# Kernel tuning notes

Hardware: AMD Instinct MI355X
Metric: run time of the kernel (lower is better)

## Reference

```python
import jax, jax.numpy as jnp
import numpy as np

B, T, D, K = 64, 512, 1024, 50


def setup_inputs() -> dict:
    key = jax.random.key(0)
    ks = jax.random.split(key, 6)
    inputs = jax.random.normal(ks[0], (B, T, D), dtype=jnp.float32)
    mask = jnp.ones((B, T), dtype=jnp.int32)
    labels = jax.random.randint(ks[1], (B, T), 0, K)
    W = jax.random.normal(ks[2], (D, K), dtype=jnp.float32) / jnp.sqrt(jnp.float32(D))
    b = jnp.zeros((K,), dtype=jnp.float32)
    transitions = jax.random.normal(ks[3], (K, K), dtype=jnp.float32) * 0.1
    start_transitions = jax.random.normal(ks[4], (K,), dtype=jnp.float32) * 0.1
    end_transitions = jax.random.normal(ks[5], (K,), dtype=jnp.float32) * 0.1
    return dict(inputs=inputs, mask=mask, labels=labels, W=W, b=b,
                transitions=transitions, start_transitions=start_transitions,
                end_transitions=end_transitions)


def _log_partition(emissions, mask_f, trans, start, end):
    # emissions [B,T,K]; forward algorithm with logsumexp recurrence (lax.scan)
    alpha0 = start[None, :] + emissions[:, 0]  # [B,K]
    def step(alpha, xs):
        emit, m = xs  # [B,K], [B]
        inner = alpha[:, :, None] + trans[None, :, :] + emit[:, None, :]  # [B,K,K]
        new = jax.nn.logsumexp(inner, axis=1)
        alpha = jnp.where(m[:, None] > 0, new, alpha)  # carry state through padding
        return alpha, None
    emits = jnp.swapaxes(emissions[:, 1:], 0, 1)  # [T-1,B,K]
    ms = jnp.swapaxes(mask_f[:, 1:], 0, 1)
    alpha, _ = jax.lax.scan(step, alpha0, (emits, ms))
    return jax.nn.logsumexp(alpha + end[None, :], axis=1)  # [B]


def _gold_score(emissions, labels, mask_f, trans, start, end):
    emit_sc = jnp.take_along_axis(emissions, labels[..., None], axis=2)[..., 0]  # [B,T]
    emit_sum = jnp.sum(emit_sc * mask_f, axis=1)
    trans_sc = trans[labels[:, :-1], labels[:, 1:]]  # [B,T-1]
    trans_sum = jnp.sum(trans_sc * mask_f[:, 1:], axis=1)
    last_idx = jnp.sum(mask_f, axis=1).astype(jnp.int32) - 1
    last_tags = jnp.take_along_axis(labels, last_idx[:, None], axis=1)[:, 0]
    return start[labels[:, 0]] + emit_sum + trans_sum + end[last_tags]


def _viterbi(emissions, mask_f, trans, start, end):
    Bv, Tv, Kv = emissions.shape
    alpha0 = start[None, :] + emissions[:, 0]
    ident = jnp.broadcast_to(jnp.arange(Kv, dtype=jnp.int32)[None, :], (Bv, Kv))
    def step(alpha, xs):
        emit, m = xs
        inner = alpha[:, :, None] + trans[None, :, :]  # [B,K_prev,K_cur]
        bp = jnp.argmax(inner, axis=1).astype(jnp.int32)  # [B,K]
        new = jnp.max(inner, axis=1) + emit
        cond = m[:, None] > 0
        alpha = jnp.where(cond, new, alpha)
        bp = jnp.where(cond, bp, ident)  # padded step: tag carries through
        return alpha, bp
    emits = jnp.swapaxes(emissions[:, 1:], 0, 1)
    ms = jnp.swapaxes(mask_f[:, 1:], 0, 1)
    alpha, bps = jax.lax.scan(step, alpha0, (emits, ms))  # bps [T-1,B,K]
    last = jnp.argmax(alpha + end[None, :], axis=1).astype(jnp.int32)  # [B]
    def back(tag, bp):
        prev = jnp.take_along_axis(bp, tag[:, None], axis=1)[:, 0]
        return prev, tag
    first_tag, tags_rest = jax.lax.scan(back, last, bps, reverse=True)  # tags_rest[t]=tag at pos t+1
    tags = jnp.concatenate([first_tag[None, :], tags_rest], axis=0)  # [T,B]
    return jnp.swapaxes(tags, 0, 1)  # [B,T]


def reference(inputs, mask, labels, W, b, transitions, start_transitions, end_transitions):
    emissions = inputs @ W + b  # tag_projection: [B,T,K]
    mask_f = mask.astype(emissions.dtype)
    scores = emissions * mask_f[..., None]  # module masks logits before CRF
    tags = _viterbi(scores, mask_f, transitions, start_transitions, end_transitions)
    tags = tags * mask.astype(tags.dtype)
    ll = _gold_score(scores, labels, mask_f, transitions, start_transitions, end_transitions) \
         - _log_partition(scores, mask_f, transitions, start_transitions, end_transitions)
    loss = -jnp.sum(ll)  # reduction='sum' negative log-likelihood
    return scores, tags, loss
```

## Files before the change

### kernel.cpp

```cpp
#include <hip/hip_runtime.h>

#define B_ 64
#define T_ 512
#define D_ 1024
#define K_ 50
#define MROWS (B_ * T_)

__global__ __launch_bounds__(256) void gemm_kernel(const float* __restrict__ A,
                                                   const float* __restrict__ W,
                                                   float* __restrict__ P0,
                                                   float* __restrict__ P1) {
  __shared__ float As[128][20];
  __shared__ float Wt[52][20];

  const int tid = threadIdx.x;
  const int rowBase = blockIdx.x * 128;
  const int kBase = blockIdx.y * 512;
  float* __restrict__ P = blockIdx.y ? P1 : P0;

  const int rg = tid & 63;
  const int cg = tid >> 6;
  const int c0 = cg * 13;
  const int swr = (rg >> 3) & 3;

  float acc[2][13];
#pragma unroll
  for (int i = 0; i < 2; i++)
#pragma unroll
    for (int j = 0; j < 13; j++) acc[i][j] = 0.f;

  const int q = tid & 3;
  const int rr = tid >> 2;

  for (int ch = 0; ch < 32; ++ch) {
    const int kb = kBase + (ch << 4);
#pragma unroll
    for (int s = 0; s < 2; s++) {
      const int r = rr + 64 * s;
      const float4 v = *(const float4*)&A[(size_t)(rowBase + r) * 1024 + kb + q * 4];
      const int p = (q + ((r >> 3) & 3)) & 3;
      *(float4*)&As[r][p * 4] = v;
    }
#pragma unroll
    for (int s = 0; s < 4; s++) {
      const int l = tid + 256 * s;
      if (l < 832) {
        const int kk = l / 52;
        const int c = l - kk * 52;
        Wt[c][kk] = (c < 50) ? W[(size_t)(kb + kk) * 50 + c] : 0.f;
      }
    }
    __syncthreads();
#pragma unroll
    for (int k4 = 0; k4 < 4; k4++) {
      const int pq = ((k4 + swr) & 3) * 4;
      const float4 a0 = *(const float4*)&As[rg][pq];
      const float4 a1 = *(const float4*)&As[rg + 64][pq];
#pragma unroll
      for (int j = 0; j < 13; j++) {
        const float4 w = *(const float4*)&Wt[c0 + j][k4 * 4];
        float t0 = acc[0][j], t1 = acc[1][j];
        t0 = fmaf(a0.x, w.x, t0); t1 = fmaf(a1.x, w.x, t1);
        t0 = fmaf(a0.y, w.y, t0); t1 = fmaf(a1.y, w.y, t1);
        t0 = fmaf(a0.z, w.z, t0); t1 = fmaf(a1.z, w.z, t1);
        t0 = fmaf(a0.w, w.w, t0); t1 = fmaf(a1.w, w.w, t1);
        acc[0][j] = t0; acc[1][j] = t1;
      }
    }
    __syncthreads();
  }
#pragma unroll
  for (int j = 0; j < 13; j++) {
    const int c = c0 + j;
    if (c < 50) {
      P[(size_t)(rowBase + rg) * 50 + c] = acc[0][j];
      P[(size_t)(rowBase + rg + 64) * 50 + c] = acc[1][j];
    }
  }
}

__global__ __launch_bounds__(256) void combine_kernel(const float* __restrict__ P1,
                                                      const float* __restrict__ bias,
                                                      const int* __restrict__ mask,
                                                      float* __restrict__ scores,
                                                      float* __restrict__ lossSlot) {
  const int idx = blockIdx.x * 256 + threadIdx.x;
  const int m = idx / 50;
  const int c = idx - m * 50;
  const float v = (scores[idx] + P1[idx] + bias[c]) * (float)mask[m];
  scores[idx] = v;
  if (idx == 0) *lossSlot = 0.f;
}

__global__ __launch_bounds__(256) void crf_kernel(const float* __restrict__ scores,
                                                  const int* __restrict__ mask,
                                                  const int* __restrict__ labels,
                                                  const float* __restrict__ trans,
                                                  const float* __restrict__ startT,
                                                  const float* __restrict__ endT,
                                                  float* __restrict__ tagsOut,
                                                  float* __restrict__ lossSlot) {
  __shared__ float x_lds[64];
  __shared__ unsigned char bp_s[511 * 52];
  __shared__ unsigned char g_s[32 * 52];
  __shared__ unsigned char chin_s[32];
  __shared__ float redp_s[4];
  __shared__ int redm_s[4];
  __shared__ float logZ_s;
  __shared__ int last_s;

  const int b = blockIdx.x;
  const int tid = threadIdx.x;
  const int wave = tid >> 6;
  const int lane = tid & 63;
  const int k = lane;
  const int kc = (k < 50) ? k : 49;
  const size_t sb = (size_t)b * T_ * 50;
  const int bT = b * T_;

  if (blockIdx.y == 0) {
    if (wave == 0) {
      float4 eTv[13];
#pragma unroll
      for (int u = 0; u < 13; u++) {
        const int j = 4 * u;
        eTv[u].x = (j + 0 < 50) ? __expf(trans[(j + 0) * 50 + kc]) : 0.f;
        eTv[u].y = (j + 1 < 50) ? __expf(trans[(j + 1) * 50 + kc]) : 0.f;
        eTv[u].z = (j + 2 < 50) ? __expf(trans[(j + 2) * 50 + kc]) : 0.f;
        eTv[u].w = (j + 3 < 50) ? __expf(trans[(j + 3) * 50 + kc]) : 0.f;
      }
      float af = (k < 50) ? (startT[k] + scores[sb + k]) : -1e30f;
      float M = __int_as_float(__builtin_amdgcn_readfirstlane(__float_as_int(af)));
      float em0 = scores[sb + 50 + kc];
      float em1 = scores[sb + 100 + kc];
      int mk0 = mask[bT + 1];
      int mk1 = mask[bT + 2];
      for (int t = 1; t < T_; ++t) {
        const float emit = em0;
        const int mt = mk0;
        em0 = em1; mk0 = mk1;
        if (t + 2 < T_) {
          em1 = scores[sb + (size_t)(t + 2) * 50 + kc];
          mk1 = mask[bT + t + 2];
        }
        const float e = __expf(af - M);
        x_lds[lane] = e;
        float p0 = 0.f, p1 = 0.f, p2 = 0.f, p3 = 0.f;
#pragma unroll
        for (int u = 0; u < 13; u++) {
          const float4 w = *(const float4*)&x_lds[4 * u];
          p0 = fmaf(w.x, eTv[u].x, p0);
          p1 = fmaf(w.y, eTv[u].y, p1);
          p2 = fmaf(w.z, eTv[u].z, p2);
          p3 = fmaf(w.w, eTv[u].w, p3);
        }
        const float S = (p0 + p1) + (p2 + p3);
        const float afn = M + __logf(S) + emit;
        af = (mt > 0 && k < 50) ? afn : af;
        M = __int_as_float(__builtin_amdgcn_readfirstlane(__float_as_int(af)));
      }
      const float x = (k < 50) ? (af + endT[k]) : -3e38f;
      float mx = x;
#pragma unroll
      for (int off = 32; off >= 1; off >>= 1) mx = fmaxf(mx, __shfl_xor(mx, off));
      float sm = (k < 50) ? __expf(x - mx) : 0.f;
#pragma unroll
      for (int off = 32; off >= 1; off >>= 1) sm += __shfl_xor(sm, off);
      if (lane == 0) logZ_s = mx + __logf(sm);
    } else {
      float part = 0.f;
      int mcnt = 0;
#pragma unroll
      for (int s = 0; s < 3; s++) {
        const int t = (tid - 64) + 192 * s;
        if (t < T_) {
          const int lt = labels[bT + t];
          const int mt = mask[bT + t];
          mcnt += mt;
          if (mt > 0) part += scores[sb + (size_t)t * 50 + lt];
          if (t < T_ - 1) {
            const int ln = labels[bT + t + 1];
            const int mn = mask[bT + t + 1];
            if (mn > 0) part += trans[lt * 50 + ln];
          }
        }
      }
#pragma unroll
      for (int off = 32; off >= 1; off >>= 1) {
        part += __shfl_xor(part, off);
        mcnt += __shfl_xor(mcnt, off);
      }
      if (lane == 0) { redp_s[wave] = part; redm_s[wave] = mcnt; }
    }
    __syncthreads();
    if (tid == 0) {
      float gold = redp_s[1] + redp_s[2] + redp_s[3];
      const int tot = redm_s[1] + redm_s[2] + redm_s[3];
      const int l0 = labels[bT];
      const int llast = labels[bT + (tot - 1)];
      gold += startT[l0] + endT[llast];
      atomicAdd(lossSlot, -(gold - logZ_s));
    }
  } else {
    if (wave == 0) {
      float4 Tv[13];
#pragma unroll
      for (int u = 0; u < 13; u++) {
        const int j = 4 * u;
        Tv[u].x = (j + 0 < 50) ? trans[(j + 0) * 50 + kc] : -1e30f;
        Tv[u].y = (j + 1 < 50) ? trans[(j + 1) * 50 + kc] : -1e30f;
        Tv[u].z = (j + 2 < 50) ? trans[(j + 2) * 50 + kc] : -1e30f;
        Tv[u].w = (j + 3 < 50) ? trans[(j + 3) * 50 + kc] : -1e30f;
      }
      float av = (k < 50) ? (startT[k] + scores[sb + k]) : -1e30f;
      float em0 = scores[sb + 50 + kc];
      float em1 = scores[sb + 100 + kc];
      int mk0 = mask[bT + 1];
      int mk1 = mask[bT + 2];
      for (int t = 1; t < T_; ++t) {
        const float emit = em0;
        const int mt = mk0;
        em0 = em1; mk0 = mk1;
        if (t + 2 < T_) {
          em1 = scores[sb + (size_t)(t + 2) * 50 + kc];
          mk1 = mask[bT + t + 2];
        }
        x_lds[lane] = av;
        float4 u0, u1, u2, u3, u4, u5, u6, u7, u8, u9, u10, u11, u12;
        float m13[13];
#define VIT_QUAD(Q, UQ)                                            \
        {                                                          \
          const float4 w = *(const float4*)&x_lds[4 * (Q)];        \
          UQ.x = w.x + Tv[Q].x; UQ.y = w.y + Tv[Q].y;              \
          UQ.z = w.z + Tv[Q].z; UQ.w = w.w + Tv[Q].w;              \
          m13[Q] = fmaxf(fmaxf(UQ.x, UQ.y), fmaxf(UQ.z, UQ.w));    \
        }
        VIT_QUAD(0, u0)   VIT_QUAD(1, u1)   VIT_QUAD(2, u2)
        VIT_QUAD(3, u3)   VIT_QUAD(4, u4)   VIT_QUAD(5, u5)
        VIT_QUAD(6, u6)   VIT_QUAD(7, u7)   VIT_QUAD(8, u8)
        VIT_QUAD(9, u9)   VIT_QUAD(10, u10) VIT_QUAD(11, u11)
        VIT_QUAD(12, u12)
#undef VIT_QUAD
        const float h0 = fmaxf(m13[0], m13[1]);
        const float h1 = fmaxf(m13[2], m13[3]);
        const float h2 = fmaxf(m13[4], m13[5]);
        const float h3 = fmaxf(m13[6], m13[7]);
        const float h4 = fmaxf(m13[8], m13[9]);
        const float h5 = fmaxf(m13[10], m13[11]);
        const float best = fmaxf(fmaxf(fmaxf(h0, h1), fmaxf(h2, h3)),
                                 fmaxf(fmaxf(h4, h5), m13[12]));
        int bj = 0;
#define VIT_SCAN(Q, UQ)                                   \
        bj = (UQ.w == best) ? 4 * (Q) + 3 : bj;           \
        bj = (UQ.z == best) ? 4 * (Q) + 2 : bj;           \
        bj = (UQ.y == best) ? 4 * (Q) + 1 : bj;           \
        bj = (UQ.x == best) ? 4 * (Q) + 0 : bj;
        VIT_SCAN(12, u12) VIT_SCAN(11, u11) VIT_SCAN(10, u10)
        VIT_SCAN(9, u9)   VIT_SCAN(8, u8)   VIT_SCAN(7, u7)
        VIT_SCAN(6, u6)   VIT_SCAN(5, u5)   VIT_SCAN(4, u4)
        VIT_SCAN(3, u3)   VIT_SCAN(2, u2)   VIT_SCAN(1, u1)
        VIT_SCAN(0, u0)
#undef VIT_SCAN
        if (k < 50) bp_s[(t - 1) * 52 + k] = (unsigned char)((mt > 0) ? bj : k);
        av = (mt > 0 && k < 50) ? (best + emit) : av;
      }
      float x = (k < 50) ? (av + endT[k]) : -3e38f;
      int xi = (k < 50) ? k : 63;
#pragma unroll
      for (int off = 32; off >= 1; off >>= 1) {
        const float ov = __shfl_xor(x, off);
        const int oi = __shfl_xor(xi, off);
        if (ov > x || (ov == x && oi < xi)) { x = ov; xi = oi; }
      }
      if (lane == 0) last_s = xi;
    }
    __syncthreads();
    const int last = last_s;
    for (int p = 0; p < 7; p++) {
      const int idx = tid + 256 * p;
      if (idx < 1600) {
        const int c = idx / 50;
        const int s2 = idx - c * 50;
        int x2 = s2;
        const int lo = 16 * c;
        const int hi = min(16 * c + 15, 510);
        for (int i = hi; i >= lo; --i) x2 = bp_s[i * 52 + x2];
        g_s[c * 52 + s2] = (unsigned char)x2;
      }
    }
    __syncthreads();
    if (tid == 0) {
      int cur = last;
      chin_s[31] = (unsigned char)cur;
      for (int c = 31; c >= 1; --c) {
        cur = g_s[c * 52 + cur];
        chin_s[c - 1] = (unsigned char)cur;
      }
      const int m511 = mask[bT + 511];
      tagsOut[(size_t)bT + 511] = (float)((m511 > 0) ? last : 0);
    }
    __syncthreads();
    if (tid < 32) {
      const int c = tid;
      int x3 = chin_s[c];
      const int lo = 16 * c;
      const int hi = min(16 * c + 15, 510);
      for (int i = hi; i >= lo; --i) {
        x3 = bp_s[i * 52 + x3];
        const int mi = mask[bT + i];
        tagsOut[(size_t)bT + i] = (float)((mi > 0) ? x3 : 0);
      }
    }
  }
}

extern "C" void kernel_launch(void* const* d_in, const int* in_sizes, int n_in,
                              void* d_out, int out_size, void* d_ws, size_t ws_size,
                              hipStream_t stream) {
  const float* inputs = (const float*)d_in[0];
  const int* mask = (const int*)d_in[1];
  const int* labels = (const int*)d_in[2];
  const float* W = (const float*)d_in[3];
  const float* bias = (const float*)d_in[4];
  const float* trans = (const float*)d_in[5];
  const float* startT = (const float*)d_in[6];
  const float* endT = (const float*)d_in[7];

  float* out = (float*)d_out;
  float* scores = out;
  float* tagsOut = out + (size_t)B_ * T_ * K_;
  float* lossSlot = out + (size_t)B_ * T_ * K_ + B_ * T_;
  float* P1 = (float*)d_ws;

  dim3 g1(MROWS / 128, 2);
  gemm_kernel<<<g1, 256, 0, stream>>>(inputs, W, scores, P1);

  combine_kernel<<<(K_ * MROWS) / 256, 256, 0, stream>>>(P1, bias, mask, scores,
                                                         lossSlot);

  dim3 g3(B_, 2);
  crf_kernel<<<g3, 256, 0, stream>>>(scores, mask, labels, trans, startT, endT,
                                     tagsOut, lossSlot);
}
```

Before: 663.9 us.

## Retile GEMM to 4x7 per thread with register prefetch; split CRF into single-wave blocks

The GEMM now gives each thread 4 rows by 7 columns instead of 2 by 13, which changes the mix of LDS reads and FMAs. Global loads for the next k-chunk are prefetched into registers so their latency overlaps the current chunk's compute. The CRF kernel now launches one 64-thread wave per block, and the gold-score reduction moves to its own third block row that adds its contribution to the loss atomically. The forward and Viterbi waves no longer share a block with idle waves, and transition vectors are pinned in registers with inline asm, at the cost of more total blocks and one more atomic per batch row.

```diff
diff --git a/kernel.cpp b/kernel.cpp
--- a/kernel.cpp
+++ b/kernel.cpp
@@ -18,63 +18,86 @@
   const int kBase = blockIdx.y * 512;
   float* __restrict__ P = blockIdx.y ? P1 : P0;
 
-  const int rg = tid & 63;
-  const int cg = tid >> 6;
-  const int c0 = cg * 13;
+  const int rg = tid & 31;
+  const int cg = tid >> 5;
+  const int c0 = cg * 7;
   const int swr = (rg >> 3) & 3;
-
-  float acc[2][13];
-#pragma unroll
-  for (int i = 0; i < 2; i++)
-#pragma unroll
-    for (int j = 0; j < 13; j++) acc[i][j] = 0.f;
 
   const int q = tid & 3;
   const int rr = tid >> 2;
+  const int pA0 = ((q + ((rr >> 3) & 3)) & 3) * 4;
+  const int pA1 = ((q + (((rr + 64) >> 3) & 3)) & 3) * 4;
+  const int kk0 = tid / 52,         cw0 = tid - kk0 * 52;
+  const int kk1 = (tid + 256) / 52, cw1 = tid + 256 - kk1 * 52;
+  const int kk2 = (tid + 512) / 52, cw2 = tid + 512 - kk2 * 52;
+  const int kk3 = (tid + 768) / 52, cw3 = tid + 768 - kk3 * 52;
+
+  float acc[4][7];
+#pragma unroll
+  for (int i = 0; i < 4; i++)
+#pragma unroll
+    for (int j = 0; j < 7; j++) acc[i][j] = 0.f;
+
+  const float* __restrict__ pA0g = &A[(size_t)(rowBase + rr) * 1024 + kBase + q * 4];
+  const float* __restrict__ pA1g = &A[(size_t)(rowBase + rr + 64) * 1024 + kBase + q * 4];
+  const float* __restrict__ pWg = &W[(size_t)kBase * 50];
+
+  float4 nA0 = *(const float4*)pA0g;
+  float4 nA1 = *(const float4*)pA1g;
+  float nW0 = (cw0 < 50) ? pWg[(size_t)kk0 * 50 + cw0] : 0.f;
+  float nW1 = (cw1 < 50) ? pWg[(size_t)kk1 * 50 + cw1] : 0.f;
+  float nW2 = (cw2 < 50) ? pWg[(size_t)kk2 * 50 + cw2] : 0.f;
+  float nW3 = (tid < 64 && cw3 < 50) ? pWg[(size_t)kk3 * 50 + cw3] : 0.f;
 
   for (int ch = 0; ch < 32; ++ch) {
-    const int kb = kBase + (ch << 4);
-#pragma unroll
-    for (int s = 0; s < 2; s++) {
-      const int r = rr + 64 * s;
-      const float4 v = *(const float4*)&A[(size_t)(rowBase + r) * 1024 + kb + q * 4];
-      const int p = (q + ((r >> 3) & 3)) & 3;
-      *(float4*)&As[r][p * 4] = v;
-    }
-#pragma unroll
-    for (int s = 0; s < 4; s++) {
-      const int l = tid + 256 * s;
-      if (l < 832) {
-        const int kk = l / 52;
-        const int c = l - kk * 52;
-        Wt[c][kk] = (c < 50) ? W[(size_t)(kb + kk) * 50 + c] : 0.f;
-      }
-    }
-    __syncthreads();
+    *(float4*)&As[rr][pA0] = nA0;
+    *(float4*)&As[rr + 64][pA1] = nA1;
+    Wt[cw0][kk0] = nW0;
+    Wt[cw1][kk1] = nW1;
+    Wt[cw2][kk2] = nW2;
+    if (tid < 64) Wt[cw3][kk3] = nW3;
+    __syncthreads();
+    if (ch < 31) {
+      const int off = (ch + 1) * 16;
+      nA0 = *(const float4*)(pA0g + off);
+      nA1 = *(const float4*)(pA1g + off);
+      const float* pw = pWg + (size_t)off * 50;
+      nW0 = (cw0 < 50) ? pw[(size_t)kk0 * 50 + cw0] : 0.f;
+      nW1 = (cw1 < 50) ? pw[(size_t)kk1 * 50 + cw1] : 0.f;
+      nW2 = (cw2 < 50) ? pw[(size_t)kk2 * 50 + cw2] : 0.f;
+      nW3 = (tid < 64 && cw3 < 50) ? pw[(size_t)kk3 * 50 + cw3] : 0.f;
+    }
 #pragma unroll
     for (int k4 = 0; k4 < 4; k4++) {
       const int pq = ((k4 + swr) & 3) * 4;
       const float4 a0 = *(const float4*)&As[rg][pq];
-      const float4 a1 = *(const float4*)&As[rg + 64][pq];
-#pragma unroll
-      for (int j = 0; j < 13; j++) {
+      const float4 a1 = *(const float4*)&As[rg + 32][pq];
+      const float4 a2 = *(const float4*)&As[rg + 64][pq];
+      const float4 a3 = *(const float4*)&As[rg + 96][pq];
+#pragma unroll
+      for (int j = 0; j < 7; j++) {
         const float4 w = *(const float4*)&Wt[c0 + j][k4 * 4];
-        float t0 = acc[0][j], t1 = acc[1][j];
+        float t0 = acc[0][j], t1 = acc[1][j], t2 = acc[2][j], t3 = acc[3][j];
         t0 = fmaf(a0.x, w.x, t0); t1 = fmaf(a1.x, w.x, t1);
+        t2 = fmaf(a2.x, w.x, t2); t3 = fmaf(a3.x, w.x, t3);
         t0 = fmaf(a0.y, w.y, t0); t1 = fmaf(a1.y, w.y, t1);
+        t2 = fmaf(a2.y, w.y, t2); t3 = fmaf(a3.y, w.y, t3);
         t0 = fmaf(a0.z, w.z, t0); t1 = fmaf(a1.z, w.z, t1);
+        t2 = fmaf(a2.z, w.z, t2); t3 = fmaf(a3.z, w.z, t3);
         t0 = fmaf(a0.w, w.w, t0); t1 = fmaf(a1.w, w.w, t1);
-        acc[0][j] = t0; acc[1][j] = t1;
+        t2 = fmaf(a2.w, w.w, t2); t3 = fmaf(a3.w, w.w, t3);
+        acc[0][j] = t0; acc[1][j] = t1; acc[2][j] = t2; acc[3][j] = t3;
       }
     }
     __syncthreads();
   }
 #pragma unroll
-  for (int j = 0; j < 13; j++) {
+  for (int j = 0; j < 7; j++) {
     const int c = c0 + j;
     if (c < 50) {
-      P[(size_t)(rowBase + rg) * 50 + c] = acc[0][j];
-      P[(size_t)(rowBase + rg + 64) * 50 + c] = acc[1][j];
+#pragma unroll
+      for (int i = 0; i < 4; i++)
+        P[(size_t)(rowBase + rg + 32 * i) * 50 + c] = acc[i][j];
     }
   }
 }
@@ -92,204 +115,163 @@
   if (idx == 0) *lossSlot = 0.f;
 }
 
-__global__ __launch_bounds__(256) void crf_kernel(const float* __restrict__ scores,
-                                                  const int* __restrict__ mask,
-                                                  const int* __restrict__ labels,
-                                                  const float* __restrict__ trans,
-                                                  const float* __restrict__ startT,
-                                                  const float* __restrict__ endT,
-                                                  float* __restrict__ tagsOut,
-                                                  float* __restrict__ lossSlot) {
+#define PIN4(V) asm volatile("" : "+v"(V.x), "+v"(V.y), "+v"(V.z), "+v"(V.w))
+
+__global__ __launch_bounds__(64, 1) void crf_kernel(const float* __restrict__ scores,
+                                                    const int* __restrict__ mask,
+                                                    const int* __restrict__ labels,
+                                                    const float* __restrict__ trans,
+                                                    const float* __restrict__ startT,
+                                                    const float* __restrict__ endT,
+                                                    float* __restrict__ tagsOut,
+                                                    float* __restrict__ lossSlot) {
   __shared__ float x_lds[64];
   __shared__ unsigned char bp_s[511 * 52];
   __shared__ unsigned char g_s[32 * 52];
   __shared__ unsigned char chin_s[32];
-  __shared__ float redp_s[4];
-  __shared__ int redm_s[4];
-  __shared__ float logZ_s;
-  __shared__ int last_s;
 
   const int b = blockIdx.x;
-  const int tid = threadIdx.x;
-  const int wave = tid >> 6;
-  const int lane = tid & 63;
+  const int lane = threadIdx.x;
   const int k = lane;
   const int kc = (k < 50) ? k : 49;
   const size_t sb = (size_t)b * T_ * 50;
   const int bT = b * T_;
 
   if (blockIdx.y == 0) {
-    if (wave == 0) {
-      float4 eTv[13];
+    float4 eTv[13];
+#pragma unroll
+    for (int u = 0; u < 13; u++) {
+      const int j = 4 * u;
+      eTv[u].x = (j + 0 < 50) ? __expf(trans[(j + 0) * 50 + kc]) : 0.f;
+      eTv[u].y = (j + 1 < 50) ? __expf(trans[(j + 1) * 50 + kc]) : 0.f;
+      eTv[u].z = (j + 2 < 50) ? __expf(trans[(j + 2) * 50 + kc]) : 0.f;
+      eTv[u].w = (j + 3 < 50) ? __expf(trans[(j + 3) * 50 + kc]) : 0.f;
+      PIN4(eTv[u]);
+    }
+    float af = (k < 50) ? (startT[k] + scores[sb + k]) : -1e30f;
+    float M = __int_as_float(__builtin_amdgcn_readfirstlane(__float_as_int(af)));
+    float em0 = scores[sb + 50 + kc];
+    float em1 = scores[sb + 100 + kc];
+    int mk0 = mask[bT + 1];
+    int mk1 = mask[bT + 2];
+    for (int t = 1; t < T_; ++t) {
+      const float emit = em0;
+      const int mt = mk0;
+      em0 = em1; mk0 = mk1;
+      if (t + 2 < T_) {
+        em1 = scores[sb + (size_t)(t + 2) * 50 + kc];
+        mk1 = mask[bT + t + 2];
+      }
+      const float e = __expf(af - M);
+      x_lds[lane] = e;
+      float p0 = 0.f, p1 = 0.f, p2 = 0.f, p3 = 0.f;
 #pragma unroll
       for (int u = 0; u < 13; u++) {
-        const int j = 4 * u;
-        eTv[u].x = (j + 0 < 50) ? __expf(trans[(j + 0) * 50 + kc]) : 0.f;
-        eTv[u].y = (j + 1 < 50) ? __expf(trans[(j + 1) * 50 + kc]) : 0.f;
-        eTv[u].z = (j + 2 < 50) ? __expf(trans[(j + 2) * 50 + kc]) : 0.f;
-        eTv[u].w = (j + 3 < 50) ? __expf(trans[(j + 3) * 50 + kc]) : 0.f;
-      }
-      float af = (k < 50) ? (startT[k] + scores[sb + k]) : -1e30f;
-      float M = __int_as_float(__builtin_amdgcn_readfirstlane(__float_as_int(af)));
-      float em0 = scores[sb + 50 + kc];
-      float em1 = scores[sb + 100 + kc];
-      int mk0 = mask[bT + 1];
-      int mk1 = mask[bT + 2];
-      for (int t = 1; t < T_; ++t) {
-        const float emit = em0;
-        const int mt = mk0;
-        em0 = em1; mk0 = mk1;
-        if (t + 2 < T_) {
-          em1 = scores[sb + (size_t)(t + 2) * 50 + kc];
-          mk1 = mask[bT + t + 2];
-        }
-        const float e = __expf(af - M);
-        x_lds[lane] = e;
-        float p0 = 0.f, p1 = 0.f, p2 = 0.f, p3 = 0.f;
-#pragma unroll
-        for (int u = 0; u < 13; u++) {
-          const float4 w = *(const float4*)&x_lds[4 * u];
-          p0 = fmaf(w.x, eTv[u].x, p0);
-          p1 = fmaf(w.y, eTv[u].y, p1);
-          p2 = fmaf(w.z, eTv[u].z, p2);
-          p3 = fmaf(w.w, eTv[u].w, p3);
-        }
-        const float S = (p0 + p1) + (p2 + p3);
-        const float afn = M + __logf(S) + emit;
-        af = (mt > 0 && k < 50) ? afn : af;
-        M = __int_as_float(__builtin_amdgcn_readfirstlane(__float_as_int(af)));
-      }
-      const float x = (k < 50) ? (af + endT[k]) : -3e38f;
-      float mx = x;
-#pragma unroll
-      for (int off = 32; off >= 1; off >>= 1) mx = fmaxf(mx, __shfl_xor(mx, off));
-      float sm = (k < 50) ? __expf(x - mx) : 0.f;
-#pragma unroll
-      for (int off = 32; off >= 1; off >>= 1) sm += __shfl_xor(sm, off);
-      if (lane == 0) logZ_s = mx + __logf(sm);
-    } else {
-      float part = 0.f;
-      int mcnt = 0;
-#pragma unroll
-      for (int s = 0; s < 3; s++) {
-        const int t = (tid - 64) + 192 * s;
-        if (t < T_) {
-          const int lt = labels[bT + t];
-          const int mt = mask[bT + t];
-          mcnt += mt;
-          if (mt > 0) part += scores[sb + (size_t)t * 50 + lt];
-          if (t < T_ - 1) {
-            const int ln = labels[bT + t + 1];
-            const int mn = mask[bT + t + 1];
-            if (mn > 0) part += trans[lt * 50 + ln];
-          }
-        }
-      }
-#pragma unroll
-      for (int off = 32; off >= 1; off >>= 1) {
-        part += __shfl_xor(part, off);
-        mcnt += __shfl_xor(mcnt, off);
-      }
-      if (lane == 0) { redp_s[wave] = part; redm_s[wave] = mcnt; }
-    }
-    __syncthreads();
-    if (tid == 0) {
-      float gold = redp_s[1] + redp_s[2] + redp_s[3];
-      const int tot = redm_s[1] + redm_s[2] + redm_s[3];
-      const int l0 = labels[bT];
-      const int llast = labels[bT + (tot - 1)];
-      gold += startT[l0] + endT[llast];
-      atomicAdd(lossSlot, -(gold - logZ_s));
-    }
-  } else {
-    if (wave == 0) {
-      float4 Tv[13];
-#pragma unroll
-      for (int u = 0; u < 13; u++) {
-        const int j = 4 * u;
-        Tv[u].x = (j + 0 < 50) ? trans[(j + 0) * 50 + kc] : -1e30f;
-        Tv[u].y = (j + 1 < 50) ? trans[(j + 1) * 50 + kc] : -1e30f;
-        Tv[u].z = (j + 2 < 50) ? trans[(j + 2) * 50 + kc] : -1e30f;
-        Tv[u].w = (j + 3 < 50) ? trans[(j + 3) * 50 + kc] : -1e30f;
-      }
-      float av = (k < 50) ? (startT[k] + scores[sb + k]) : -1e30f;
-      float em0 = scores[sb + 50 + kc];
-      float em1 = scores[sb + 100 + kc];
-      int mk0 = mask[bT + 1];
-      int mk1 = mask[bT + 2];
-      for (int t = 1; t < T_; ++t) {
-        const float emit = em0;
-        const int mt = mk0;
-        em0 = em1; mk0 = mk1;
-        if (t + 2 < T_) {
-          em1 = scores[sb + (size_t)(t + 2) * 50 + kc];
-          mk1 = mask[bT + t + 2];
-        }
-        x_lds[lane] = av;
-        float4 u0, u1, u2, u3, u4, u5, u6, u7, u8, u9, u10, u11, u12;
-        float m13[13];
+        const float4 w = *(const float4*)&x_lds[4 * u];
+        p0 = fmaf(w.x, eTv[u].x, p0);
+        p1 = fmaf(w.y, eTv[u].y, p1);
+        p2 = fmaf(w.z, eTv[u].z, p2);
+        p3 = fmaf(w.w, eTv[u].w, p3);
+      }
+      const float S = (p0 + p1) + (p2 + p3);
+      const float afn = M + __logf(S) + emit;
+      af = (mt > 0 && k < 50) ? afn : af;
+      M = __int_as_float(__builtin_amdgcn_readfirstlane(__float_as_int(af)));
+    }
+    const float x = (k < 50) ? (af + endT[k]) : -3e38f;
+    float mx = x;
+#pragma unroll
+    for (int off = 32; off >= 1; off >>= 1) mx = fmaxf(mx, __shfl_xor(mx, off));
+    float sm = (k < 50) ? __expf(x - mx) : 0.f;
+#pragma unroll
+    for (int off = 32; off >= 1; off >>= 1) sm += __shfl_xor(sm, off);
+    if (lane == 0) atomicAdd(lossSlot, mx + __logf(sm));
+  } else if (blockIdx.y == 1) {
+    float4 Tv[13];
+#pragma unroll
+    for (int u = 0; u < 13; u++) {
+      const int j = 4 * u;
+      Tv[u].x = (j + 0 < 50) ? trans[(j + 0) * 50 + kc] : -1e30f;
+      Tv[u].y = (j + 1 < 50) ? trans[(j + 1) * 50 + kc] : -1e30f;
+      Tv[u].z = (j + 2 < 50) ? trans[(j + 2) * 50 + kc] : -1e30f;
+      Tv[u].w = (j + 3 < 50) ? trans[(j + 3) * 50 + kc] : -1e30f;
+      PIN4(Tv[u]);
+    }
+    float av = (k < 50) ? (startT[k] + scores[sb + k]) : -1e30f;
+    float em0 = scores[sb + 50 + kc];
+    float em1 = scores[sb + 100 + kc];
+    int mk0 = mask[bT + 1];
+    int mk1 = mask[bT + 2];
+    for (int t = 1; t < T_; ++t) {
+      const float emit = em0;
+      const int mt = mk0;
+      em0 = em1; mk0 = mk1;
+      if (t + 2 < T_) {
+        em1 = scores[sb + (size_t)(t + 2) * 50 + kc];
+        mk1 = mask[bT + t + 2];
+      }
+      x_lds[lane] = av;
+      float4 u0, u1, u2, u3, u4, u5, u6, u7, u8, u9, u10, u11, u12;
+      float m13[13];
 #define VIT_QUAD(Q, UQ)                                            \
-        {                                                          \
-          const float4 w = *(const float4*)&x_lds[4 * (Q)];        \
-          UQ.x = w.x + Tv[Q].x; UQ.y = w.y + Tv[Q].y;              \
-          UQ.z = w.z + Tv[Q].z; UQ.w = w.w + Tv[Q].w;              \
-          m13[Q] = fmaxf(fmaxf(UQ.x, UQ.y), fmaxf(UQ.z, UQ.w));    \
-        }
-        VIT_QUAD(0, u0)   VIT_QUAD(1, u1)   VIT_QUAD(2, u2)
-        VIT_QUAD(3, u3)   VIT_QUAD(4, u4)   VIT_QUAD(5, u5)
-        VIT_QUAD(6, u6)   VIT_QUAD(7, u7)   VIT_QUAD(8, u8)
-        VIT_QUAD(9, u9)   VIT_QUAD(10, u10) VIT_QUAD(11, u11)
-        VIT_QUAD(12, u12)
+      {                                                            \
+        const float4 w = *(const float4*)&x_lds[4 * (Q)];          \
+        UQ.x = w.x + Tv[Q].x; UQ.y = w.y + Tv[Q].y;                \
+        UQ.z = w.z + Tv[Q].z; UQ.w = w.w + Tv[Q].w;                \
+        m13[Q] = fmaxf(fmaxf(UQ.x, UQ.y), fmaxf(UQ.z, UQ.w));      \
+      }
+      VIT_QUAD(0, u0)   VIT_QUAD(1, u1)   VIT_QUAD(2, u2)
+      VIT_QUAD(3, u3)   VIT_QUAD(4, u4)   VIT_QUAD(5, u5)
+      VIT_QUAD(6, u6)   VIT_QUAD(7, u7)   VIT_QUAD(8, u8)
+      VIT_QUAD(9, u9)   VIT_QUAD(10, u10) VIT_QUAD(11, u11)
+      VIT_QUAD(12, u12)
 #undef VIT_QUAD
-        const float h0 = fmaxf(m13[0], m13[1]);
-        const float h1 = fmaxf(m13[2], m13[3]);
-        const float h2 = fmaxf(m13[4], m13[5]);
-        const float h3 = fmaxf(m13[6], m13[7]);
-        const float h4 = fmaxf(m13[8], m13[9]);
-        const float h5 = fmaxf(m13[10], m13[11]);
-        const float best = fmaxf(fmaxf(fmaxf(h0, h1), fmaxf(h2, h3)),
-                                 fmaxf(fmaxf(h4, h5), m13[12]));
-        int bj = 0;
+      const float h0 = fmaxf(m13[0], m13[1]);
+      const float h1 = fmaxf(m13[2], m13[3]);
+      const float h2 = fmaxf(m13[4], m13[5]);
+      const float h3 = fmaxf(m13[6], m13[7]);
+      const float h4 = fmaxf(m13[8], m13[9]);
+      const float h5 = fmaxf(m13[10], m13[11]);
+      const float best = fmaxf(fmaxf(fmaxf(h0, h1), fmaxf(h2, h3)),
+                               fmaxf(fmaxf(h4, h5), m13[12]));
+      int bj = 0;
 #define VIT_SCAN(Q, UQ)                                   \
-        bj = (UQ.w == best) ? 4 * (Q) + 3 : bj;           \
-        bj = (UQ.z == best) ? 4 * (Q) + 2 : bj;           \
-        bj = (UQ.y == best) ? 4 * (Q) + 1 : bj;           \
-        bj = (UQ.x == best) ? 4 * (Q) + 0 : bj;
-        VIT_SCAN(12, u12) VIT_SCAN(11, u11) VIT_SCAN(10, u10)
-        VIT_SCAN(9, u9)   VIT_SCAN(8, u8)   VIT_SCAN(7, u7)
-        VIT_SCAN(6, u6)   VIT_SCAN(5, u5)   VIT_SCAN(4, u4)
-        VIT_SCAN(3, u3)   VIT_SCAN(2, u2)   VIT_SCAN(1, u1)
-        VIT_SCAN(0, u0)
+      bj = (UQ.w == best) ? 4 * (Q) + 3 : bj;             \
+      bj = (UQ.z == best) ? 4 * (Q) + 2 : bj;             \
+      bj = (UQ.y == best) ? 4 * (Q) + 1 : bj;             \
+      bj = (UQ.x == best) ? 4 * (Q) + 0 : bj;
+      VIT_SCAN(12, u12) VIT_SCAN(11, u11) VIT_SCAN(10, u10)
+      VIT_SCAN(9, u9)   VIT_SCAN(8, u8)   VIT_SCAN(7, u7)
+      VIT_SCAN(6, u6)   VIT_SCAN(5, u5)   VIT_SCAN(4, u4)
+      VIT_SCAN(3, u3)   VIT_SCAN(2, u2)   VIT_SCAN(1, u1)
+      VIT_SCAN(0, u0)
 #undef VIT_SCAN
-        if (k < 50) bp_s[(t - 1) * 52 + k] = (unsigned char)((mt > 0) ? bj : k);
-        av = (mt > 0 && k < 50) ? (best + emit) : av;
-      }
-      float x = (k < 50) ? (av + endT[k]) : -3e38f;
-      int xi = (k < 50) ? k : 63;
-#pragma unroll
-      for (int off = 32; off >= 1; off >>= 1) {
-        const float ov = __shfl_xor(x, off);
-        const int oi = __shfl_xor(xi, off);
-        if (ov > x || (ov == x && oi < xi)) { x = ov; xi = oi; }
-      }
-      if (lane == 0) last_s = xi;
-    }
-    __syncthreads();
-    const int last = last_s;
-    for (int p = 0; p < 7; p++) {
-      const int idx = tid + 256 * p;
-      if (idx < 1600) {
-        const int c = idx / 50;
-        const int s2 = idx - c * 50;
-        int x2 = s2;
-        const int lo = 16 * c;
-        const int hi = min(16 * c + 15, 510);
-        for (int i = hi; i >= lo; --i) x2 = bp_s[i * 52 + x2];
-        g_s[c * 52 + s2] = (unsigned char)x2;
-      }
-    }
-    __syncthreads();
-    if (tid == 0) {
+      if (k < 50) bp_s[(t - 1) * 52 + k] = (unsigned char)((mt > 0) ? bj : k);
+      av = (mt > 0 && k < 50) ? (best + emit) : av;
+    }
+    float x = (k < 50) ? (av + endT[k]) : -3e38f;
+    int xi = (k < 50) ? k : 63;
+#pragma unroll
+    for (int off = 32; off >= 1; off >>= 1) {
+      const float ov = __shfl_xor(x, off);
+      const int oi = __shfl_xor(xi, off);
+      if (ov > x || (ov == x && oi < xi)) { x = ov; xi = oi; }
+    }
+    const int last = xi;
+    __syncthreads();
+#pragma unroll 1
+    for (int p = 0; p < 25; p++) {
+      const int idx = lane + 64 * p;
+      const int c = idx / 50;
+      const int s2 = idx - c * 50;
+      int x2 = s2;
+      const int lo = 16 * c;
+      const int hi = min(16 * c + 15, 510);
+      for (int i = hi; i >= lo; --i) x2 = bp_s[i * 52 + x2];
+      g_s[c * 52 + s2] = (unsigned char)x2;
+    }
+    __syncthreads();
+    if (lane == 0) {
       int cur = last;
       chin_s[31] = (unsigned char)cur;
       for (int c = 31; c >= 1; --c) {
@@ -300,8 +282,8 @@
       tagsOut[(size_t)bT + 511] = (float)((m511 > 0) ? last : 0);
     }
     __syncthreads();
-    if (tid < 32) {
-      const int c = tid;
+    if (lane < 32) {
+      const int c = lane;
       int x3 = chin_s[c];
       const int lo = 16 * c;
       const int hi = min(16 * c + 15, 510);
@@ -310,6 +292,33 @@
         const int mi = mask[bT + i];
         tagsOut[(size_t)bT + i] = (float)((mi > 0) ? x3 : 0);
       }
+    }
+  } else {
+    float part = 0.f;
+    int mcnt = 0;
+#pragma unroll
+    for (int s = 0; s < 8; s++) {
+      const int t = lane + 64 * s;
+      const int lt = labels[bT + t];
+      const int mt = mask[bT + t];
+      mcnt += mt;
+      if (mt > 0) part += scores[sb + (size_t)t * 50 + lt];
+      if (t < T_ - 1) {
+        const int ln = labels[bT + t + 1];
+        const int mn = mask[bT + t + 1];
+        if (mn > 0) part += trans[lt * 50 + ln];
+      }
+    }
+#pragma unroll
+    for (int off = 32; off >= 1; off >>= 1) {
+      part += __shfl_xor(part, off);
+      mcnt += __shfl_xor(mcnt, off);
+    }
+    if (lane == 0) {
+      const int l0 = labels[bT];
+      const int llast = labels[bT + (mcnt - 1)];
+      const float gold = part + startT[l0] + endT[llast];
+      atomicAdd(lossSlot, -gold);
     }
   }
 }
@@ -338,7 +347,7 @@
   combine_kernel<<<(K_ * MROWS) / 256, 256, 0, stream>>>(P1, bias, mask, scores,
                                                          lossSlot);
 
-  dim3 g3(B_, 2);
-  crf_kernel<<<g3, 256, 0, stream>>>(scores, mask, labels, trans, startT, endT,
-                                     tagsOut, lossSlot);
+  dim3 g3(B_, 3);
+  crf_kernel<<<g3, 64, 0, stream>>>(scores, mask, labels, trans, startT, endT,
+                                    tagsOut, lossSlot);
 }
```

Measured after the change: 610.4 us. 8.1% less time.
